# Performance work log

Measured on AMD Instinct MI355X. Metric: run time of the kernel, lower is better.

The kernel has to match this reference:

```python
import jax, jax.numpy as jnp
import numpy as np

T = 0.2  # temperature

def setup_inputs() -> dict:
    key = jax.random.key(0)
    k1, k2 = jax.random.split(key)
    l_enc = jax.random.normal(k1, (1024, 128, 256), dtype=jnp.float32)
    g_enc = jax.random.normal(k2, (1024, 256), dtype=jnp.float32)
    return {"l_enc": l_enc, "g_enc": g_enc}

def reference(l_enc, g_enc):
    num_assign = l_enc.shape[1]
    l2 = l_enc.reshape(-1, l_enc.shape[-1])           # [N, C], N = B*num_assign
    x_abs = jnp.linalg.norm(l2, axis=1)               # [N]
    g_abs = jnp.linalg.norm(g_enc, axis=1)            # [K]
    # positive pairs: each local row vs its own graph embedding
    g_expand = jnp.repeat(g_enc, num_assign, axis=0)  # [N, C]
    g_expand_abs = jnp.repeat(g_abs, num_assign)      # [N]
    l_pos = jnp.einsum('nc,nc->n', l2, g_expand) / (x_abs * g_expand_abs)
    l_pos = jnp.exp(l_pos / T)                        # [N]
    # full similarity: cosine sim of every local row vs every graph embedding
    sim = jnp.einsum('nc,kc->nk', l2, g_enc) / (x_abs[:, None] * g_abs[None, :])
    sim = jnp.exp(sim / T)                            # [N, K]
    loss = l_pos / (sim.sum(axis=1) - l_pos)
    return -jnp.mean(jnp.log(loss))
```

## Files before the change

kernel.cpp:

```cpp
#include <hip/hip_runtime.h>
#include <hip/hip_bf16.h>
#include <stdint.h>

typedef __bf16 bf16x8 __attribute__((ext_vector_type(8)));
typedef float  f32x16 __attribute__((ext_vector_type(16)));

#define K2EXP 7.2134752044448170f
#define LN2F  0.6931471805599453f

__device__ __forceinline__ unsigned short f2bf(float f) {
  __bf16 h = (__bf16)f;
  return __builtin_bit_cast(unsigned short, h);
}

__global__ __launch_bounds__(256) void k_ghat(const float* __restrict__ g,
                                              char* __restrict__ ghat) {
  const int w = threadIdx.x >> 6, l = threadIdx.x & 63;
  const int row = blockIdx.x * 4 + w;
  const float4 v = *(const float4*)(g + (size_t)row * 256 + l * 4);
  float s = v.x * v.x + v.y * v.y + v.z * v.z + v.w * v.w;
  #pragma unroll
  for (int m = 1; m <= 32; m <<= 1) s += __shfl_xor(s, m, 64);
  const float rn = rsqrtf(s);
  ushort4 o;
  o.x = f2bf(v.x * rn); o.y = f2bf(v.y * rn);
  o.z = f2bf(v.z * rn); o.w = f2bf(v.w * rn);
  const int off = row * 512 + ((l * 8) ^ ((row & 31) << 4));
  *(ushort4*)(ghat + off) = o;
}

__global__ __launch_bounds__(256)
__attribute__((amdgpu_waves_per_eu(2)))
void k_main(const float* __restrict__ l2,
            const char* __restrict__ ghat,
            float* __restrict__ out) {
  __shared__ __align__(16) char smem[2 * 32768 + 512 + 64];
  float* posl = (float*)(smem + 65536);
  float* bsum = (float*)(smem + 65536 + 512);

  const int tid = threadIdx.x;
  const int w   = tid >> 6;
  const int l   = tid & 63;
  const int lm  = l & 31;
  const int lh  = l >> 5;
  const int wrb = blockIdx.x * 128 + w * 32;
  const int p   = blockIdx.x;
  const int pc  = p >> 6;
  const int pf  = (p >> 5) & 1;

  if (tid == 0) *bsum = 0.f;

  auto stage = [&](int c, int buf) {
    const char* gsrc = ghat + c * 32768 + w * 1024 + l * 16;
    char* ldst = smem + buf * 32768 + w * 1024;
    #pragma unroll
    for (int i = 0; i < 8; ++i) {
      __builtin_amdgcn_global_load_lds(
          (const __attribute__((address_space(1))) void*)(gsrc + i * 4096),
          (__attribute__((address_space(3))) void*)(ldst + i * 4096),
          16, 0, 0);
    }
  };

  stage(0, 0);

  bf16x8 af0, af1, af2, af3, af4, af5, af6, af7,
         af8, af9, af10, af11, af12, af13, af14, af15;
  float ssq = 0.f;
  const float* rp = l2 + (size_t)(wrb + lm) * 256 + lh * 8;

#define LOADA(s) { \
    const float4 a = *(const float4*)(rp + (s) * 16); \
    const float4 b = *(const float4*)(rp + (s) * 16 + 4); \
    ssq += a.x*a.x + a.y*a.y + a.z*a.z + a.w*a.w \
         + b.x*b.x + b.y*b.y + b.z*b.z + b.w*b.w; \
    bf16x8 f; \
    f[0] = (__bf16)a.x; f[1] = (__bf16)a.y; f[2] = (__bf16)a.z; f[3] = (__bf16)a.w; \
    f[4] = (__bf16)b.x; f[5] = (__bf16)b.y; f[6] = (__bf16)b.z; f[7] = (__bf16)b.w; \
    af##s = f; }

  LOADA(0) LOADA(1) LOADA(2) LOADA(3)
  __builtin_amdgcn_sched_barrier(0);
  LOADA(4) LOADA(5) LOADA(6) LOADA(7)
  __builtin_amdgcn_sched_barrier(0);
  LOADA(8) LOADA(9) LOADA(10) LOADA(11)
  __builtin_amdgcn_sched_barrier(0);
  LOADA(12) LOADA(13) LOADA(14) LOADA(15)
#undef LOADA

  const float rn = rsqrtf(ssq + __shfl_xor(ssq, 32, 64));
#define NRM(s) { bf16x8 f = af##s; \
    f[0] = (__bf16)((float)f[0] * rn); f[1] = (__bf16)((float)f[1] * rn); \
    f[2] = (__bf16)((float)f[2] * rn); f[3] = (__bf16)((float)f[3] * rn); \
    f[4] = (__bf16)((float)f[4] * rn); f[5] = (__bf16)((float)f[5] * rn); \
    f[6] = (__bf16)((float)f[6] * rn); f[7] = (__bf16)((float)f[7] * rn); \
    af##s = f; }
  NRM(0) NRM(1) NRM(2) NRM(3) NRM(4) NRM(5) NRM(6) NRM(7)
  NRM(8) NRM(9) NRM(10) NRM(11) NRM(12) NRM(13) NRM(14) NRM(15)
#undef NRM

  float rs0 = 0.f, rs1 = 0.f, rs2 = 0.f, rs3 = 0.f,
        rs4 = 0.f, rs5 = 0.f, rs6 = 0.f, rs7 = 0.f,
        rs8 = 0.f, rs9 = 0.f, rs10 = 0.f, rs11 = 0.f,
        rs12 = 0.f, rs13 = 0.f, rs14 = 0.f, rs15 = 0.f;

  __syncthreads();

#define MSTEP(s) { \
    const uint4 raw = *(const uint4*)(base + col_l * 512 + (((s) * 32 + lh * 16) ^ sw)); \
    acc = __builtin_amdgcn_mfma_f32_32x32x16_bf16( \
              af##s, __builtin_bit_cast(bf16x8, raw), acc, 0, 0, 0); }
#define ESTEP(j) rs##j += __builtin_amdgcn_exp2f(acc[j] * K2EXP);

  for (int c = 0; c < 16; ++c) {
    if (c < 15) stage(c + 1, (c + 1) & 1);
    const char* base = smem + (c & 1) * 32768;
    #pragma unroll
    for (int cf = 0; cf < 2; ++cf) {
      const int col_l = cf * 32 + lm;
      const int sw = (col_l & 31) << 4;
      f32x16 acc = {0.f};
      MSTEP(0)  MSTEP(1)  MSTEP(2)  MSTEP(3)
      MSTEP(4)  MSTEP(5)  MSTEP(6)  MSTEP(7)
      MSTEP(8)  MSTEP(9)  MSTEP(10) MSTEP(11)
      MSTEP(12) MSTEP(13) MSTEP(14) MSTEP(15)
      ESTEP(0)  ESTEP(1)  ESTEP(2)  ESTEP(3)
      ESTEP(4)  ESTEP(5)  ESTEP(6)  ESTEP(7)
      ESTEP(8)  ESTEP(9)  ESTEP(10) ESTEP(11)
      ESTEP(12) ESTEP(13) ESTEP(14) ESTEP(15)
      if (c == pc && cf == pf && lm == (p & 31)) {
        #pragma unroll
        for (int j = 0; j < 16; ++j) {
          const int r0 = (j & 3) + 8 * (j >> 2) + 4 * lh;
          posl[w * 32 + r0] = acc[j] * K2EXP;
        }
      }
    }
    __syncthreads();
  }
#undef MSTEP
#undef ESTEP

#define RED(j) { float v = rs##j; \
    v += __shfl_xor(v, 1, 64); v += __shfl_xor(v, 2, 64); \
    v += __shfl_xor(v, 4, 64); v += __shfl_xor(v, 8, 64); \
    v += __shfl_xor(v, 16, 64); rs##j = v; }
  RED(0) RED(1) RED(2) RED(3) RED(4) RED(5) RED(6) RED(7)
  RED(8) RED(9) RED(10) RED(11) RED(12) RED(13) RED(14) RED(15)
#undef RED

  if (lm == 0) {
    float local = 0.f;
#define FIN(j) { \
    const int r0 = ((j) & 3) + 8 * ((j) >> 2) + 4 * lh; \
    const float cs = posl[w * 32 + r0]; \
    const float S  = rs##j - __builtin_amdgcn_exp2f(cs); \
    local += (__builtin_amdgcn_logf(S) - cs) * LN2F; }
    FIN(0) FIN(1) FIN(2) FIN(3) FIN(4) FIN(5) FIN(6) FIN(7)
    FIN(8) FIN(9) FIN(10) FIN(11) FIN(12) FIN(13) FIN(14) FIN(15)
#undef FIN
    atomicAdd(bsum, local);
  }
  __syncthreads();
  if (tid == 0) atomicAdd(out, *bsum * (1.0f / 131072.0f));
}

extern "C" void kernel_launch(void* const* d_in, const int* in_sizes, int n_in,
                              void* d_out, int out_size, void* d_ws, size_t ws_size,
                              hipStream_t stream) {
  (void)in_sizes; (void)n_in; (void)out_size; (void)ws_size;
  const float* l2 = (const float*)d_in[0];
  const float* g  = (const float*)d_in[1];
  float* out = (float*)d_out;

  char* ghat = (char*)d_ws;

  hipMemsetAsync(d_out, 0, sizeof(float), stream);
  k_ghat<<<256, 256, 0, stream>>>(g, ghat);
  k_main<<<1024, 256, 0, stream>>>(l2, ghat, out);
}
```

Baseline: 93.44 us.

## Process 64 rows per wave to reuse each LDS B fragment twice

Each wave now holds A fragments for two 32-row groups and issues two MFMAs per B fragment read from LDS. This halves LDS reads and global-to-LDS staging of the normalized graph embeddings per row. Each block covers 256 rows, so the grid drops to 512 blocks. The cost is double the register footprint for A fragments, accumulators and row sums, so the occupancy hint is lowered to 1 wave per EU. That may reduce latency hiding for the input loads and the exp work.

```diff
diff --git a/kernel.cpp b/kernel.cpp
--- a/kernel.cpp
+++ b/kernel.cpp
@@ -30,28 +30,28 @@
 }
 
 __global__ __launch_bounds__(256)
-__attribute__((amdgpu_waves_per_eu(2)))
+__attribute__((amdgpu_waves_per_eu(1)))
 void k_main(const float* __restrict__ l2,
             const char* __restrict__ ghat,
             float* __restrict__ out) {
-  __shared__ __align__(16) char smem[2 * 32768 + 512 + 64];
+  __shared__ __align__(16) char smem[2 * 32768 + 1024 + 64];
   float* posl = (float*)(smem + 65536);
-  float* bsum = (float*)(smem + 65536 + 512);
+  float* bsum = (float*)(smem + 65536 + 1024);
 
   const int tid = threadIdx.x;
   const int w   = tid >> 6;
   const int l   = tid & 63;
   const int lm  = l & 31;
   const int lh  = l >> 5;
-  const int wrb = blockIdx.x * 128 + w * 32;
-  const int p   = blockIdx.x;
+  const int wrb = blockIdx.x * 256 + w * 64;
+  const int p   = blockIdx.x * 2 + (w >> 1);
   const int pc  = p >> 6;
   const int pf  = (p >> 5) & 1;
 
   if (tid == 0) *bsum = 0.f;
 
   auto stage = [&](int c, int buf) {
-    const char* gsrc = ghat + c * 32768 + w * 1024 + l * 16;
+    const char* gsrc = ghat + c * 32768 + tid * 16;
     char* ldst = smem + buf * 32768 + w * 1024;
     #pragma unroll
     for (int i = 0; i < 8; ++i) {
@@ -64,53 +64,73 @@
 
   stage(0, 0);
 
-  bf16x8 af0, af1, af2, af3, af4, af5, af6, af7,
-         af8, af9, af10, af11, af12, af13, af14, af15;
-  float ssq = 0.f;
-  const float* rp = l2 + (size_t)(wrb + lm) * 256 + lh * 8;
-
-#define LOADA(s) { \
-    const float4 a = *(const float4*)(rp + (s) * 16); \
-    const float4 b = *(const float4*)(rp + (s) * 16 + 4); \
-    ssq += a.x*a.x + a.y*a.y + a.z*a.z + a.w*a.w \
-         + b.x*b.x + b.y*b.y + b.z*b.z + b.w*b.w; \
+  bf16x8 af0_0, af0_1, af0_2,  af0_3,  af0_4,  af0_5,  af0_6,  af0_7,
+         af0_8, af0_9, af0_10, af0_11, af0_12, af0_13, af0_14, af0_15;
+  bf16x8 af1_0, af1_1, af1_2,  af1_3,  af1_4,  af1_5,  af1_6,  af1_7,
+         af1_8, af1_9, af1_10, af1_11, af1_12, af1_13, af1_14, af1_15;
+  float ssq0 = 0.f, ssq1 = 0.f;
+  const float* rp0 = l2 + (size_t)(wrb + lm) * 256 + lh * 8;
+  const float* rp1 = l2 + (size_t)(wrb + 32 + lm) * 256 + lh * 8;
+
+#define LOADA(g, s) { \
+    const float4 a = *(const float4*)(rp##g + (s) * 16); \
+    const float4 b = *(const float4*)(rp##g + (s) * 16 + 4); \
+    ssq##g += a.x*a.x + a.y*a.y + a.z*a.z + a.w*a.w \
+            + b.x*b.x + b.y*b.y + b.z*b.z + b.w*b.w; \
     bf16x8 f; \
     f[0] = (__bf16)a.x; f[1] = (__bf16)a.y; f[2] = (__bf16)a.z; f[3] = (__bf16)a.w; \
     f[4] = (__bf16)b.x; f[5] = (__bf16)b.y; f[6] = (__bf16)b.z; f[7] = (__bf16)b.w; \
-    af##s = f; }
-
-  LOADA(0) LOADA(1) LOADA(2) LOADA(3)
-  __builtin_amdgcn_sched_barrier(0);
-  LOADA(4) LOADA(5) LOADA(6) LOADA(7)
-  __builtin_amdgcn_sched_barrier(0);
-  LOADA(8) LOADA(9) LOADA(10) LOADA(11)
-  __builtin_amdgcn_sched_barrier(0);
-  LOADA(12) LOADA(13) LOADA(14) LOADA(15)
+    af##g##_##s = f; }
+
+  LOADA(0, 0) LOADA(0, 1) LOADA(0, 2) LOADA(0, 3)
+  __builtin_amdgcn_sched_barrier(0);
+  LOADA(0, 4) LOADA(0, 5) LOADA(0, 6) LOADA(0, 7)
+  __builtin_amdgcn_sched_barrier(0);
+  LOADA(0, 8) LOADA(0, 9) LOADA(0, 10) LOADA(0, 11)
+  __builtin_amdgcn_sched_barrier(0);
+  LOADA(0, 12) LOADA(0, 13) LOADA(0, 14) LOADA(0, 15)
+  __builtin_amdgcn_sched_barrier(0);
+  LOADA(1, 0) LOADA(1, 1) LOADA(1, 2) LOADA(1, 3)
+  __builtin_amdgcn_sched_barrier(0);
+  LOADA(1, 4) LOADA(1, 5) LOADA(1, 6) LOADA(1, 7)
+  __builtin_amdgcn_sched_barrier(0);
+  LOADA(1, 8) LOADA(1, 9) LOADA(1, 10) LOADA(1, 11)
+  __builtin_amdgcn_sched_barrier(0);
+  LOADA(1, 12) LOADA(1, 13) LOADA(1, 14) LOADA(1, 15)
 #undef LOADA
 
-  const float rn = rsqrtf(ssq + __shfl_xor(ssq, 32, 64));
-#define NRM(s) { bf16x8 f = af##s; \
-    f[0] = (__bf16)((float)f[0] * rn); f[1] = (__bf16)((float)f[1] * rn); \
-    f[2] = (__bf16)((float)f[2] * rn); f[3] = (__bf16)((float)f[3] * rn); \
-    f[4] = (__bf16)((float)f[4] * rn); f[5] = (__bf16)((float)f[5] * rn); \
-    f[6] = (__bf16)((float)f[6] * rn); f[7] = (__bf16)((float)f[7] * rn); \
-    af##s = f; }
-  NRM(0) NRM(1) NRM(2) NRM(3) NRM(4) NRM(5) NRM(6) NRM(7)
-  NRM(8) NRM(9) NRM(10) NRM(11) NRM(12) NRM(13) NRM(14) NRM(15)
+  const float rn0 = rsqrtf(ssq0 + __shfl_xor(ssq0, 32, 64));
+  const float rn1 = rsqrtf(ssq1 + __shfl_xor(ssq1, 32, 64));
+#define NRM(g, s) { bf16x8 f = af##g##_##s; \
+    f[0] = (__bf16)((float)f[0] * rn##g); f[1] = (__bf16)((float)f[1] * rn##g); \
+    f[2] = (__bf16)((float)f[2] * rn##g); f[3] = (__bf16)((float)f[3] * rn##g); \
+    f[4] = (__bf16)((float)f[4] * rn##g); f[5] = (__bf16)((float)f[5] * rn##g); \
+    f[6] = (__bf16)((float)f[6] * rn##g); f[7] = (__bf16)((float)f[7] * rn##g); \
+    af##g##_##s = f; }
+  NRM(0, 0) NRM(0, 1) NRM(0, 2)  NRM(0, 3)  NRM(0, 4)  NRM(0, 5)  NRM(0, 6)  NRM(0, 7)
+  NRM(0, 8) NRM(0, 9) NRM(0, 10) NRM(0, 11) NRM(0, 12) NRM(0, 13) NRM(0, 14) NRM(0, 15)
+  NRM(1, 0) NRM(1, 1) NRM(1, 2)  NRM(1, 3)  NRM(1, 4)  NRM(1, 5)  NRM(1, 6)  NRM(1, 7)
+  NRM(1, 8) NRM(1, 9) NRM(1, 10) NRM(1, 11) NRM(1, 12) NRM(1, 13) NRM(1, 14) NRM(1, 15)
 #undef NRM
 
-  float rs0 = 0.f, rs1 = 0.f, rs2 = 0.f, rs3 = 0.f,
-        rs4 = 0.f, rs5 = 0.f, rs6 = 0.f, rs7 = 0.f,
-        rs8 = 0.f, rs9 = 0.f, rs10 = 0.f, rs11 = 0.f,
-        rs12 = 0.f, rs13 = 0.f, rs14 = 0.f, rs15 = 0.f;
+  float rs0_0 = 0.f, rs0_1 = 0.f, rs0_2 = 0.f, rs0_3 = 0.f,
+        rs0_4 = 0.f, rs0_5 = 0.f, rs0_6 = 0.f, rs0_7 = 0.f,
+        rs0_8 = 0.f, rs0_9 = 0.f, rs0_10 = 0.f, rs0_11 = 0.f,
+        rs0_12 = 0.f, rs0_13 = 0.f, rs0_14 = 0.f, rs0_15 = 0.f;
+  float rs1_0 = 0.f, rs1_1 = 0.f, rs1_2 = 0.f, rs1_3 = 0.f,
+        rs1_4 = 0.f, rs1_5 = 0.f, rs1_6 = 0.f, rs1_7 = 0.f,
+        rs1_8 = 0.f, rs1_9 = 0.f, rs1_10 = 0.f, rs1_11 = 0.f,
+        rs1_12 = 0.f, rs1_13 = 0.f, rs1_14 = 0.f, rs1_15 = 0.f;
 
   __syncthreads();
 
 #define MSTEP(s) { \
     const uint4 raw = *(const uint4*)(base + col_l * 512 + (((s) * 32 + lh * 16) ^ sw)); \
-    acc = __builtin_amdgcn_mfma_f32_32x32x16_bf16( \
-              af##s, __builtin_bit_cast(bf16x8, raw), acc, 0, 0, 0); }
-#define ESTEP(j) rs##j += __builtin_amdgcn_exp2f(acc[j] * K2EXP);
+    const bf16x8 bb = __builtin_bit_cast(bf16x8, raw); \
+    acc0 = __builtin_amdgcn_mfma_f32_32x32x16_bf16(af0_##s, bb, acc0, 0, 0, 0); \
+    acc1 = __builtin_amdgcn_mfma_f32_32x32x16_bf16(af1_##s, bb, acc1, 0, 0, 0); }
+#define ESTEP(j) { rs0_##j += __builtin_amdgcn_exp2f(acc0[j] * K2EXP); \
+                   rs1_##j += __builtin_amdgcn_exp2f(acc1[j] * K2EXP); }
 
   for (int c = 0; c < 16; ++c) {
     if (c < 15) stage(c + 1, (c + 1) & 1);
@@ -119,7 +139,8 @@
     for (int cf = 0; cf < 2; ++cf) {
       const int col_l = cf * 32 + lm;
       const int sw = (col_l & 31) << 4;
-      f32x16 acc = {0.f};
+      f32x16 acc0 = {0.f};
+      f32x16 acc1 = {0.f};
       MSTEP(0)  MSTEP(1)  MSTEP(2)  MSTEP(3)
       MSTEP(4)  MSTEP(5)  MSTEP(6)  MSTEP(7)
       MSTEP(8)  MSTEP(9)  MSTEP(10) MSTEP(11)
@@ -132,7 +153,8 @@
         #pragma unroll
         for (int j = 0; j < 16; ++j) {
           const int r0 = (j & 3) + 8 * (j >> 2) + 4 * lh;
-          posl[w * 32 + r0] = acc[j] * K2EXP;
+          posl[w * 64 + r0]      = acc0[j] * K2EXP;
+          posl[w * 64 + 32 + r0] = acc1[j] * K2EXP;
         }
       }
     }
@@ -141,23 +163,27 @@
 #undef MSTEP
 #undef ESTEP
 
-#define RED(j) { float v = rs##j; \
+#define RED(g, j) { float v = rs##g##_##j; \
     v += __shfl_xor(v, 1, 64); v += __shfl_xor(v, 2, 64); \
     v += __shfl_xor(v, 4, 64); v += __shfl_xor(v, 8, 64); \
-    v += __shfl_xor(v, 16, 64); rs##j = v; }
-  RED(0) RED(1) RED(2) RED(3) RED(4) RED(5) RED(6) RED(7)
-  RED(8) RED(9) RED(10) RED(11) RED(12) RED(13) RED(14) RED(15)
+    v += __shfl_xor(v, 16, 64); rs##g##_##j = v; }
+  RED(0, 0) RED(0, 1) RED(0, 2)  RED(0, 3)  RED(0, 4)  RED(0, 5)  RED(0, 6)  RED(0, 7)
+  RED(0, 8) RED(0, 9) RED(0, 10) RED(0, 11) RED(0, 12) RED(0, 13) RED(0, 14) RED(0, 15)
+  RED(1, 0) RED(1, 1) RED(1, 2)  RED(1, 3)  RED(1, 4)  RED(1, 5)  RED(1, 6)  RED(1, 7)
+  RED(1, 8) RED(1, 9) RED(1, 10) RED(1, 11) RED(1, 12) RED(1, 13) RED(1, 14) RED(1, 15)
 #undef RED
 
   if (lm == 0) {
     float local = 0.f;
-#define FIN(j) { \
-    const int r0 = ((j) & 3) + 8 * ((j) >> 2) + 4 * lh; \
-    const float cs = posl[w * 32 + r0]; \
-    const float S  = rs##j - __builtin_amdgcn_exp2f(cs); \
+#define FIN(g, j) { \
+    const int r0 = (g) * 32 + ((j) & 3) + 8 * ((j) >> 2) + 4 * lh; \
+    const float cs = posl[w * 64 + r0]; \
+    const float S  = rs##g##_##j - __builtin_amdgcn_exp2f(cs); \
     local += (__builtin_amdgcn_logf(S) - cs) * LN2F; }
-    FIN(0) FIN(1) FIN(2) FIN(3) FIN(4) FIN(5) FIN(6) FIN(7)
-    FIN(8) FIN(9) FIN(10) FIN(11) FIN(12) FIN(13) FIN(14) FIN(15)
+    FIN(0, 0) FIN(0, 1) FIN(0, 2)  FIN(0, 3)  FIN(0, 4)  FIN(0, 5)  FIN(0, 6)  FIN(0, 7)
+    FIN(0, 8) FIN(0, 9) FIN(0, 10) FIN(0, 11) FIN(0, 12) FIN(0, 13) FIN(0, 14) FIN(0, 15)
+    FIN(1, 0) FIN(1, 1) FIN(1, 2)  FIN(1, 3)  FIN(1, 4)  FIN(1, 5)  FIN(1, 6)  FIN(1, 7)
+    FIN(1, 8) FIN(1, 9) FIN(1, 10) FIN(1, 11) FIN(1, 12) FIN(1, 13) FIN(1, 14) FIN(1, 15)
 #undef FIN
     atomicAdd(bsum, local);
   }
@@ -177,5 +203,5 @@
 
   hipMemsetAsync(d_out, 0, sizeof(float), stream);
   k_ghat<<<256, 256, 0, stream>>>(g, ghat);
-  k_main<<<1024, 256, 0, stream>>>(l2, ghat, out);
-}
+  k_main<<<512, 256, 0, stream>>>(l2, ghat, out);
+}
```

Measured after the change: 110.9 us. 1.19x slower.
